# Kernel optimization log

Measured on AMD Instinct MI355X. Metric: run time of the kernel, lower is better.

## Reference

```python
import jax, jax.numpy as jnp
import numpy as np

N_NODES = 100000
N_EDGES = 1600000
IN_DIM = 128
LATENT = [128, 128, 16]  # last entry = num classes (logits dim)


def setup_inputs() -> dict:
    key = jax.random.key(0)
    ks = jax.random.split(key, 16)
    inp = {
        "x": jax.random.normal(ks[0], (N_NODES, IN_DIM), dtype=jnp.float32),
        "edge_index": jax.random.randint(ks[1], (2, N_EDGES), 0, N_NODES, dtype=jnp.int64),
        "edge_weight": jax.random.uniform(ks[2], (N_EDGES,), dtype=jnp.float32),
    }
    dims = [IN_DIM] + LATENT
    for i in range(len(LATENT)):
        fan_in = dims[i]
        scale = 1.0 / np.sqrt(fan_in)
        inp[f"W{i}"] = jax.random.uniform(ks[3 + 2 * i], (dims[i], dims[i + 1]), minval=-scale, maxval=scale, dtype=jnp.float32)
        inp[f"b{i}"] = jax.random.uniform(ks[4 + 2 * i], (dims[i + 1],), minval=-scale, maxval=scale, dtype=jnp.float32)
        inp[f"eps{i}"] = jnp.zeros((), dtype=jnp.float32)  # GINConv train_eps init = 0
    return inp


def _gin_layer(x, W, b, eps, src, dst, edge_weight):
    # message: x_j (optionally scaled by edge weight), summed into target nodes
    msg = x[src]
    if edge_weight is not None:
        msg = msg * edge_weight[:, None]
    agg = jax.ops.segment_sum(msg, dst, num_segments=N_NODES)
    h = (1.0 + eps) * x + agg
    return jax.nn.relu(h @ W + b)  # MLP = Linear + ReLU


def _l2_normalize(x, eps=1e-12):
    norm = jnp.linalg.norm(x, axis=-1, keepdims=True)
    return x / jnp.maximum(norm, eps)


def reference(x, edge_index, edge_weight, W0, b0, eps0, W1, b1, eps1, W2, b2, eps2):
    src, dst = edge_index[0], edge_index[1]
    params = [(W0, b0, eps0), (W1, b1, eps1), (W2, b2, eps2)]
    h = x
    # all but last layer: GINConv(with edge_weight) -> l2 normalize -> ReLU
    for (W, b, e) in params[:-1]:
        h = _gin_layer(h, W, b, e, src, dst, edge_weight)
        h = _l2_normalize(h)  # emb_normlize=True
        h = jax.nn.relu(h)
    # last layer: GINConv WITHOUT edge_weight (forward passes only x, edge_index)
    W, b, e = params[-1]
    logits = _gin_layer(h, W, b, e, src, dst, None)
    probs = jax.nn.softmax(logits, axis=-1)
    return (logits, probs)
```

## Files before the change

kernel.cpp:

```cpp
#include <hip/hip_runtime.h>
#include <hip/hip_bf16.h>

#define N_NODES 100000
#define N_EDGES 1600000
#define DIM 128
#define ODIM 16
#define NB 782
#define PCHUNK 3200
#define PBLK 500
#define FCAP 2560
#define CB4 12500

typedef unsigned int uint32;
typedef float f32x2 __attribute__((ext_vector_type(2)));
typedef float f32x4 __attribute__((ext_vector_type(4)));
typedef short bf16x8 __attribute__((ext_vector_type(8)));
typedef uint32 u32x4 __attribute__((ext_vector_type(4)));
typedef uint32 u32x2 __attribute__((ext_vector_type(2)));

static __device__ __forceinline__ float bflo(uint32 p) { return __uint_as_float(p << 16); }
static __device__ __forceinline__ float bfhi(uint32 p) { return __uint_as_float(p & 0xFFFF0000u); }
static __device__ __forceinline__ unsigned short f2bf(float f) {
  __hip_bfloat16 h = __float2bfloat16(f);
  return *reinterpret_cast<unsigned short*>(&h);
}
static __device__ __forceinline__ uint32 pk2bf(float a, float b) {
  return (uint32)f2bf(a) | ((uint32)f2bf(b) << 16);
}

__global__ __launch_bounds__(256) void prep_kernel(
    const f32x4* __restrict__ x4, uint32* __restrict__ Xu,
    const float* __restrict__ W0, const float* __restrict__ W1,
    const float* __restrict__ W2,
    unsigned short* __restrict__ pW0, unsigned short* __restrict__ pW1,
    unsigned short* __restrict__ pW2,
    const int* __restrict__ dst, int* __restrict__ bcnt) {
  __shared__ int h[NB];
  int b = blockIdx.x;
  int tid = threadIdx.x;
  if (b < CB4) {
    int i = b * 256 + tid;
    f32x4 v = __builtin_nontemporal_load(x4 + i);
    u32x2 o = {pk2bf(v[0], v[1]), pk2bf(v[2], v[3])};
    *(u32x2*)(Xu + (size_t)i * 2) = o;
  } else if (b < CB4 + 128) {
    int wsel = (b - CB4) >> 6;
    int idx = ((b - CB4) & 63) * 256 + tid;
    int j = idx & 7, lane = (idx >> 3) & 63, nt = (idx >> 9) & 7, kc = idx >> 12;
    const float* W = wsel ? W1 : W0;
    unsigned short* pW = wsel ? pW1 : pW0;
    pW[idx] = f2bf(W[(kc * 32 + (lane >> 4) * 8 + j) * DIM + nt * 16 + (lane & 15)]);
  } else if (b < CB4 + 136) {
    int idx = (b - CB4 - 128) * 256 + tid;
    int j = idx & 7, lane = (idx >> 3) & 63, kc = idx >> 9;
    pW2[idx] = f2bf(W2[(kc * 32 + (lane >> 4) * 8 + j) * ODIM + (lane & 15)]);
  } else {
    for (int i = tid; i < NB; i += 256) h[i] = 0;
    __syncthreads();
    int e0 = (b - CB4 - 136) * PCHUNK;
    for (int i = tid; i < PCHUNK; i += 256)
      atomicAdd(&h[__builtin_nontemporal_load(dst + e0 + i) >> 7], 1);
    __syncthreads();
    for (int i = tid; i < NB; i += 256)
      if (h[i]) atomicAdd(&bcnt[i], h[i]);
  }
}

__global__ __launch_bounds__(512) void coarse_partition_kernel(
    const int* __restrict__ src, const int* __restrict__ dst,
    const float* __restrict__ ew, const int* __restrict__ bcnt,
    int* __restrict__ bcur, int2* __restrict__ epack) {
  __shared__ int hist[NB];
  __shared__ int base_a[NB];
  __shared__ int base_g[NB];
  __shared__ int lcur_a[NB];
  __shared__ int gbase_a[NB];
  __shared__ int2 stg[PCHUNK];
  __shared__ int gpos[PCHUNK];

  int tid = threadIdx.x;
  int e0 = blockIdx.x * PCHUNK;

  for (int i = tid; i < NB; i += 512) hist[i] = 0;
  __syncthreads();
  for (int i = tid; i < PCHUNK; i += 512) atomicAdd(&hist[dst[e0 + i] >> 7], 1);
  __syncthreads();

  if (tid < 64) {
    int run = 0, rung = 0;
#pragma unroll
    for (int c = 0; c < 13; c++) {
      int idx = c * 64 + tid;
      int v = (idx < NB) ? hist[idx] : 0;
      int vg = (idx < NB) ? bcnt[idx] : 0;
      int incl = v, inclg = vg;
#pragma unroll
      for (int off = 1; off < 64; off <<= 1) {
        int t1 = __shfl_up(incl, off, 64);
        int t2 = __shfl_up(inclg, off, 64);
        if (tid >= off) { incl += t1; inclg += t2; }
      }
      if (idx < NB) {
        base_a[idx] = run + incl - v;
        base_g[idx] = rung + inclg - vg;
      }
      run += __shfl(incl, 63, 64);
      rung += __shfl(inclg, 63, 64);
    }
  }
  __syncthreads();
  for (int i = tid; i < NB; i += 512) {
    int c = hist[i];
    gbase_a[i] = (c > 0) ? base_g[i] + atomicAdd(&bcur[i], c) : 0;
    lcur_a[i] = base_a[i];
  }
  __syncthreads();

  for (int i = tid; i < PCHUNK; i += 512) {
    int e = e0 + i;
    int s = __builtin_nontemporal_load(src + e);
    int d = dst[e];
    float w = __builtin_nontemporal_load(ew + e);
    int bkt = d >> 7;
    int pos = atomicAdd(&lcur_a[bkt], 1);
    stg[pos] = make_int2(s | ((d & 127) << 20), __float_as_int(w));
    gpos[pos] = gbase_a[bkt] + (pos - base_a[bkt]);
  }
  __syncthreads();
  for (int i = tid; i < PCHUNK; i += 512) epack[gpos[i]] = stg[i];
}

__global__ __launch_bounds__(512) void fine_sort_kernel(
    const int* __restrict__ bcnt, int2* __restrict__ epack,
    int* __restrict__ row_ptr) {
  __shared__ int2 ebuf[FCAP];
  __shared__ unsigned short inv[FCAP];
  __shared__ int hist[128];
  __shared__ int sc[128];
  __shared__ int cur[128];
  __shared__ int redc[8];
  int tid = threadIdx.x;
  int b = blockIdx.x;
  int node0 = b << 7;

  int part = 0;
  for (int i = tid; i < b; i += 512) part += bcnt[i];
#pragma unroll
  for (int off = 32; off >= 1; off >>= 1) part += __shfl_xor(part, off, 64);
  if ((tid & 63) == 0) redc[tid >> 6] = part;
  if (tid < 128) hist[tid] = 0;
  __syncthreads();
  int lo = redc[0] + redc[1] + redc[2] + redc[3] +
           redc[4] + redc[5] + redc[6] + redc[7];
  int n = bcnt[b];
  if (n > FCAP) n = FCAP;

  for (int i = tid; i < n; i += 512) {
    int2 e = epack[lo + i];
    ebuf[i] = e;
    atomicAdd(&hist[(e.x >> 20) & 127], 1);
  }
  __syncthreads();
  if (tid < 64) {
    int run = 0;
#pragma unroll
    for (int c = 0; c < 2; c++) {
      int idx = c * 64 + tid;
      int v = hist[idx];
      int incl = v;
#pragma unroll
      for (int off = 1; off < 64; off <<= 1) {
        int tv = __shfl_up(incl, off, 64);
        if (tid >= off) incl += tv;
      }
      sc[idx] = run + incl;
      run += __shfl(incl, 63, 64);
    }
  }
  __syncthreads();
  if (tid < 128) {
    int excl = sc[tid] - hist[tid];
    if (node0 + tid < N_NODES) row_ptr[node0 + tid] = lo + excl;
    cur[tid] = excl;
  }
  if (b == 0 && tid == 0) row_ptr[N_NODES] = N_EDGES;
  __syncthreads();
  for (int i = tid; i < n; i += 512) {
    int p = atomicAdd(&cur[(ebuf[i].x >> 20) & 127], 1);
    inv[p] = (unsigned short)i;
  }
  __syncthreads();
  for (int p = tid; p < n; p += 512) {
    int2 e = ebuf[inv[p]];
    epack[lo + p] = make_int2(e.x & 0xFFFFF, e.y);
  }
}

__global__ __launch_bounds__(256, 8) void gather_bf16(
    const uint32* __restrict__ hu, const int* __restrict__ row_ptr,
    const int2* __restrict__ ep, const float* __restrict__ eps_p,
    uint32* __restrict__ cg) {
  int lane = threadIdx.x & 63;
  int node = blockIdx.x * 4 + (threadIdx.x >> 6);
  if (node >= N_NODES) return;
  int grp = lane >> 4, l4 = lane & 15;
  int a = row_ptr[node], bnd = row_ptr[node + 1];
  float epf = 1.0f + *eps_p;
  uint4 xv = *(const uint4*)(hu + (size_t)node * 64 + l4 * 4);
  f32x2 acc2[4];
#pragma unroll
  for (int k = 0; k < 4; k++) acc2[k] = (f32x2){0.f, 0.f};

  auto acc8 = [&](float wv, const uint4& p) {
    acc2[0] += (f32x2){bflo(p.x), bfhi(p.x)} * wv;
    acc2[1] += (f32x2){bflo(p.y), bfhi(p.y)} * wv;
    acc2[2] += (f32x2){bflo(p.z), bfhi(p.z)} * wv;
    acc2[3] += (f32x2){bflo(p.w), bfhi(p.w)} * wv;
  };

#pragma unroll 2
  for (int j = a; j < bnd; j += 16) {
    int i0 = j + grp;
    int i1 = i0 + 4;
    int i2 = i0 + 8;
    int i3 = i0 + 12;
    int2 e0 = ep[i0 < bnd ? i0 : a];
    int2 e1 = ep[i1 < bnd ? i1 : a];
    int2 e2 = ep[i2 < bnd ? i2 : a];
    int2 e3 = ep[i3 < bnd ? i3 : a];
    uint4 p0 = *(const uint4*)(hu + (size_t)e0.x * 64 + l4 * 4);
    uint4 p1 = *(const uint4*)(hu + (size_t)e1.x * 64 + l4 * 4);
    uint4 p2 = *(const uint4*)(hu + (size_t)e2.x * 64 + l4 * 4);
    uint4 p3 = *(const uint4*)(hu + (size_t)e3.x * 64 + l4 * 4);
    float w0 = i0 < bnd ? __int_as_float(e0.y) : 0.f;
    float w1 = i1 < bnd ? __int_as_float(e1.y) : 0.f;
    float w2 = i2 < bnd ? __int_as_float(e2.y) : 0.f;
    float w3 = i3 < bnd ? __int_as_float(e3.y) : 0.f;
    acc8(w0, p0);
    acc8(w1, p1);
    acc8(w2, p2);
    acc8(w3, p3);
  }
#pragma unroll
  for (int k = 0; k < 4; k++) {
    acc2[k].x += __shfl_xor(acc2[k].x, 16, 64);
    acc2[k].x += __shfl_xor(acc2[k].x, 32, 64);
    acc2[k].y += __shfl_xor(acc2[k].y, 16, 64);
    acc2[k].y += __shfl_xor(acc2[k].y, 32, 64);
  }
  if (lane < 16) {
    u32x4 st;
    st[0] = pk2bf(fmaf(epf, bflo(xv.x), acc2[0].x), fmaf(epf, bfhi(xv.x), acc2[0].y));
    st[1] = pk2bf(fmaf(epf, bflo(xv.y), acc2[1].x), fmaf(epf, bfhi(xv.y), acc2[1].y));
    st[2] = pk2bf(fmaf(epf, bflo(xv.z), acc2[2].x), fmaf(epf, bfhi(xv.z), acc2[2].y));
    st[3] = pk2bf(fmaf(epf, bflo(xv.w), acc2[3].x), fmaf(epf, bfhi(xv.w), acc2[3].y));
    __builtin_nontemporal_store(st, (u32x4*)(cg + (size_t)node * 64 + l4 * 4));
  }
}

template <int FUSE_PROJ>
__global__ __launch_bounds__(256) void gin_mlp_mfma(
    const uint32* __restrict__ Cu,
    const unsigned char* __restrict__ pW, const float* __restrict__ b,
    uint32* outH, const unsigned char* __restrict__ pW2,
    uint32* __restrict__ yb) {
  __shared__ __align__(16) unsigned char As[64 * 272];
  int tid = threadIdx.x;
  int node0 = blockIdx.x * 64;

  const uint4* C4 = (const uint4*)Cu;
#pragma unroll
  for (int c = 0; c < 4; c++) {
    int t = c * 256 + tid;
    int n = t >> 4, s = t & 15;
    int node = node0 + n;
    int cn = node < N_NODES ? node : N_NODES - 1;
    *(uint4*)(As + n * 272 + s * 16) = C4[(size_t)cn * 16 + s];
  }
  __syncthreads();

  int w = tid >> 6, l = tid & 63;
  int m = l & 15, q = l >> 4;

  f32x4 acc[8];
#pragma unroll
  for (int nt = 0; nt < 8; nt++) acc[nt] = (f32x4){0.f, 0.f, 0.f, 0.f};

  const unsigned char* Abase = As + (w * 16 + m) * 272 + q * 16;
#pragma unroll
  for (int kc = 0; kc < 4; kc++) {
    bf16x8 af = *(const bf16x8*)(Abase + kc * 64);
#pragma unroll
    for (int nt = 0; nt < 8; nt++) {
      bf16x8 bfr = *(const bf16x8*)(pW + (size_t)((kc * 8 + nt) * 64 + l) * 16);
      acc[nt] = __builtin_amdgcn_mfma_f32_16x16x32_bf16(af, bfr, acc[nt], 0, 0, 0);
    }
  }

  float ss[4] = {0.f, 0.f, 0.f, 0.f};
#pragma unroll
  for (int nt = 0; nt < 8; nt++) {
    float bj = b[nt * 16 + m];
#pragma unroll
    for (int r = 0; r < 4; r++) {
      float v = fmaxf(acc[nt][r] + bj, 0.0f);
      acc[nt][r] = v;
      ss[r] += v * v;
    }
  }
#pragma unroll
  for (int r = 0; r < 4; r++) {
    float s = ss[r];
    s += __shfl_xor(s, 1, 64);
    s += __shfl_xor(s, 2, 64);
    s += __shfl_xor(s, 4, 64);
    s += __shfl_xor(s, 8, 64);
    ss[r] = 1.0f / fmaxf(sqrtf(s), 1e-12f);
  }
#pragma unroll
  for (int nt = 0; nt < 8; nt++) {
#pragma unroll
    for (int r = 0; r < 4; r++) {
      unsigned short hv = f2bf(acc[nt][r] * ss[r]);
      *(unsigned short*)(As + (w * 16 + q * 4 + r) * 272 + (nt * 16 + m) * 2) = hv;
    }
  }

  if (FUSE_PROJ) {
    f32x4 accy = (f32x4){0.f, 0.f, 0.f, 0.f};
#pragma unroll
    for (int kc = 0; kc < 4; kc++) {
      bf16x8 af = *(const bf16x8*)(Abase + kc * 64);
      bf16x8 bfr = *(const bf16x8*)(pW2 + (size_t)(kc * 64 + l) * 16);
      accy = __builtin_amdgcn_mfma_f32_16x16x32_bf16(af, bfr, accy, 0, 0, 0);
    }
#pragma unroll
    for (int r = 0; r < 4; r++) {
      float v = accy[r];
      float o = __shfl_xor(v, 1, 64);
      if (!(m & 1)) {
        int orow = node0 + w * 16 + q * 4 + r;
        if (orow < N_NODES) yb[(size_t)orow * 8 + (m >> 1)] = pk2bf(v, o);
      }
    }
  } else {
    __syncthreads();
    int rem = N_NODES - node0; if (rem > 64) rem = 64;
    for (int i = tid; i < 1024; i += 256) {
      int row = i >> 4, seg = i & 15;
      if (row < rem) {
        uint4 vv = *(const uint4*)(As + row * 272 + seg * 16);
        *(uint4*)((unsigned char*)outH + (size_t)(node0 + row) * 256 + seg * 16) = vv;
      }
    }
  }
}

__global__ __launch_bounds__(256) void gather16_final_kernel(
    const uint32* __restrict__ yb, const int* __restrict__ row_ptr,
    const int2* __restrict__ ep, const float* __restrict__ bb,
    const float* __restrict__ eps_p, float* __restrict__ out_logits,
    float* __restrict__ out_probs) {
  int lane = threadIdx.x & 63;
  int node = blockIdx.x * 4 + (threadIdx.x >> 6);
  if (node >= N_NODES) return;
  int f2 = lane & 3;
  int eq = lane >> 2;
  int a = row_ptr[node], bnd = row_ptr[node + 1];
  f32x4 acc = (f32x4){0.f, 0.f, 0.f, 0.f};
  for (int j = a; j < bnd; j += 16) {
    int idx = j + eq;
    int vld = idx < bnd;
    int2 e = ep[vld ? idx : a];
    u32x2 p = *(const u32x2*)(yb + (size_t)e.x * 8 + f2 * 2);
    if (vld) {
      acc[0] += bflo(p[0]); acc[1] += bfhi(p[0]);
      acc[2] += bflo(p[1]); acc[3] += bfhi(p[1]);
    }
  }
#pragma unroll
  for (int k = 0; k < 4; k++) {
#pragma unroll
    for (int off = 4; off <= 32; off <<= 1)
      acc[k] += __shfl_xor(acc[k], off, 64);
  }
  if (eq == 0) {
    float epf = 1.0f + *eps_p;
    u32x2 ys = *(const u32x2*)(yb + (size_t)node * 8 + f2 * 2);
    f32x4 lg;
    lg[0] = fmaxf(fmaf(epf, bflo(ys[0]), acc[0]) + bb[f2 * 4 + 0], 0.f);
    lg[1] = fmaxf(fmaf(epf, bfhi(ys[0]), acc[1]) + bb[f2 * 4 + 1], 0.f);
    lg[2] = fmaxf(fmaf(epf, bflo(ys[1]), acc[2]) + bb[f2 * 4 + 2], 0.f);
    lg[3] = fmaxf(fmaf(epf, bfhi(ys[1]), acc[3]) + bb[f2 * 4 + 3], 0.f);
    float mx = fmaxf(fmaxf(lg[0], lg[1]), fmaxf(lg[2], lg[3]));
    mx = fmaxf(mx, __shfl_xor(mx, 1, 4));
    mx = fmaxf(mx, __shfl_xor(mx, 2, 4));
    f32x4 ex;
    float s = 0.f;
#pragma unroll
    for (int k = 0; k < 4; k++) { ex[k] = __expf(lg[k] - mx); s += ex[k]; }
    s += __shfl_xor(s, 1, 4);
    s += __shfl_xor(s, 2, 4);
    float invs = 1.0f / s;
    size_t base = (size_t)node * ODIM + f2 * 4;
    *(f32x4*)(out_logits + base) = lg;
    f32x4 pr = {ex[0] * invs, ex[1] * invs, ex[2] * invs, ex[3] * invs};
    *(f32x4*)(out_probs + base) = pr;
  }
}

extern "C" void kernel_launch(void* const* d_in, const int* in_sizes, int n_in,
                              void* d_out, int out_size, void* d_ws, size_t ws_size,
                              hipStream_t stream) {
  const float* x = (const float*)d_in[0];
  const int* ei = (const int*)d_in[1];
  const float* ew = (const float*)d_in[2];
  const float* W0 = (const float*)d_in[3];
  const float* b0 = (const float*)d_in[4];
  const float* e0 = (const float*)d_in[5];
  const float* W1 = (const float*)d_in[6];
  const float* b1 = (const float*)d_in[7];
  const float* e1 = (const float*)d_in[8];
  const float* W2 = (const float*)d_in[9];
  const float* b2 = (const float*)d_in[10];
  const float* e2 = (const float*)d_in[11];
  float* out = (float*)d_out;

  const int* srcp = ei;
  const int* dstp = ei + N_EDGES;

  char* ws = (char*)d_ws;
  size_t off = 0;
  uint32* Cg  = (uint32*)(ws + off);  off += (size_t)N_NODES * DIM * 2;
  uint32* Xb  = (uint32*)(ws + off);  off += (size_t)N_NODES * DIM * 2;
  uint32* H   = (uint32*)(ws + off);  off += (size_t)N_NODES * DIM * 2;
  int2* epack = (int2*)(ws + off);    off += (size_t)N_EDGES * 8;
  uint32* yb  = (uint32*)(ws + off);  off += (size_t)N_NODES * 8 * 4;
  int* row_ptr = (int*)(ws + off);    off += (size_t)(N_NODES + 16) * 4;
  int* bcnt   = (int*)(ws + off);     off += 4096;
  int* bcur   = (int*)(ws + off);     off += 4096;
  unsigned short* pW0 = (unsigned short*)(ws + off); off += 32768;
  unsigned short* pW1 = (unsigned short*)(ws + off); off += 32768;
  unsigned short* pW2 = (unsigned short*)(ws + off); off += 4096;

  hipMemsetAsync(bcnt, 0, 8192, stream);
  prep_kernel<<<CB4 + 136 + PBLK, 256, 0, stream>>>(
      (const f32x4*)x, Xb, W0, W1, W2, pW0, pW1, pW2, dstp, bcnt);

  coarse_partition_kernel<<<PBLK, 512, 0, stream>>>(srcp, dstp, ew, bcnt, bcur, epack);
  fine_sort_kernel<<<NB, 512, 0, stream>>>(bcnt, epack, row_ptr);

  int ggrid = (N_NODES + 3) / 4;
  int mgrid = (N_NODES + 63) / 64;

  gather_bf16<<<ggrid, 256, 0, stream>>>(Xb, row_ptr, epack, e0, Cg);
  gin_mlp_mfma<0><<<mgrid, 256, 0, stream>>>(Cg, (const unsigned char*)pW0, b0,
                                             H, nullptr, nullptr);
  gather_bf16<<<ggrid, 256, 0, stream>>>(H, row_ptr, epack, e1, Cg);
  gin_mlp_mfma<1><<<mgrid, 256, 0, stream>>>(Cg, (const unsigned char*)pW1, b1,
                                             nullptr, (const unsigned char*)pW2, yb);
  gather16_final_kernel<<<ggrid, 256, 0, stream>>>(yb, row_ptr, epack, b2, e2,
                                                   out, out + (size_t)N_NODES * ODIM);
}
```

Before: 358.0 us.

## Replace exact bucket offsets with fixed-capacity padded buckets, dropping the histogram pass

Removes the separate per-bucket histogram pass over dst, the memset, and the global prefix sums. Instead, each coarse bucket gets a fixed slot of FCAP entries in an oversized edge buffer, and CSR uses separate row_ptr/row_end arrays. This saves a full read of dst and several scans, at the cost of a larger, sparser edge buffer. It relies on no bucket exceeding FCAP edges (overflow is silently truncated), which holds for uniform random indices but is an input-distribution assumption.

```diff
diff --git a/kernel.cpp b/kernel.cpp
--- a/kernel.cpp
+++ b/kernel.cpp
@@ -33,9 +33,7 @@
     const float* __restrict__ W0, const float* __restrict__ W1,
     const float* __restrict__ W2,
     unsigned short* __restrict__ pW0, unsigned short* __restrict__ pW1,
-    unsigned short* __restrict__ pW2,
-    const int* __restrict__ dst, int* __restrict__ bcnt) {
-  __shared__ int h[NB];
+    unsigned short* __restrict__ pW2, int* __restrict__ bcur) {
   int b = blockIdx.x;
   int tid = threadIdx.x;
   if (b < CB4) {
@@ -55,24 +53,16 @@
     int j = idx & 7, lane = (idx >> 3) & 63, kc = idx >> 9;
     pW2[idx] = f2bf(W2[(kc * 32 + (lane >> 4) * 8 + j) * ODIM + (lane & 15)]);
   } else {
-    for (int i = tid; i < NB; i += 256) h[i] = 0;
-    __syncthreads();
-    int e0 = (b - CB4 - 136) * PCHUNK;
-    for (int i = tid; i < PCHUNK; i += 256)
-      atomicAdd(&h[__builtin_nontemporal_load(dst + e0 + i) >> 7], 1);
-    __syncthreads();
-    for (int i = tid; i < NB; i += 256)
-      if (h[i]) atomicAdd(&bcnt[i], h[i]);
+    for (int i = tid; i < NB; i += 256) bcur[i] = 0;
   }
 }
 
 __global__ __launch_bounds__(512) void coarse_partition_kernel(
     const int* __restrict__ src, const int* __restrict__ dst,
-    const float* __restrict__ ew, const int* __restrict__ bcnt,
+    const float* __restrict__ ew,
     int* __restrict__ bcur, int2* __restrict__ epack) {
   __shared__ int hist[NB];
   __shared__ int base_a[NB];
-  __shared__ int base_g[NB];
   __shared__ int lcur_a[NB];
   __shared__ int gbase_a[NB];
   __shared__ int2 stg[PCHUNK];
@@ -87,31 +77,25 @@
   __syncthreads();
 
   if (tid < 64) {
-    int run = 0, rung = 0;
+    int run = 0;
 #pragma unroll
     for (int c = 0; c < 13; c++) {
       int idx = c * 64 + tid;
       int v = (idx < NB) ? hist[idx] : 0;
-      int vg = (idx < NB) ? bcnt[idx] : 0;
-      int incl = v, inclg = vg;
+      int incl = v;
 #pragma unroll
       for (int off = 1; off < 64; off <<= 1) {
         int t1 = __shfl_up(incl, off, 64);
-        int t2 = __shfl_up(inclg, off, 64);
-        if (tid >= off) { incl += t1; inclg += t2; }
+        if (tid >= off) incl += t1;
       }
-      if (idx < NB) {
-        base_a[idx] = run + incl - v;
-        base_g[idx] = rung + inclg - vg;
-      }
+      if (idx < NB) base_a[idx] = run + incl - v;
       run += __shfl(incl, 63, 64);
-      rung += __shfl(inclg, 63, 64);
     }
   }
   __syncthreads();
   for (int i = tid; i < NB; i += 512) {
     int c = hist[i];
-    gbase_a[i] = (c > 0) ? base_g[i] + atomicAdd(&bcur[i], c) : 0;
+    gbase_a[i] = (c > 0) ? i * FCAP + atomicAdd(&bcur[i], c) : 0;
     lcur_a[i] = base_a[i];
   }
   __syncthreads();
@@ -131,28 +115,21 @@
 }
 
 __global__ __launch_bounds__(512) void fine_sort_kernel(
-    const int* __restrict__ bcnt, int2* __restrict__ epack,
-    int* __restrict__ row_ptr) {
+    const int* __restrict__ bcur, int2* __restrict__ epack,
+    int* __restrict__ row_ptr, int* __restrict__ row_end) {
   __shared__ int2 ebuf[FCAP];
   __shared__ unsigned short inv[FCAP];
   __shared__ int hist[128];
   __shared__ int sc[128];
   __shared__ int cur[128];
-  __shared__ int redc[8];
   int tid = threadIdx.x;
   int b = blockIdx.x;
   int node0 = b << 7;
-
-  int part = 0;
-  for (int i = tid; i < b; i += 512) part += bcnt[i];
-#pragma unroll
-  for (int off = 32; off >= 1; off >>= 1) part += __shfl_xor(part, off, 64);
-  if ((tid & 63) == 0) redc[tid >> 6] = part;
+  int lo = b * FCAP;
+
   if (tid < 128) hist[tid] = 0;
   __syncthreads();
-  int lo = redc[0] + redc[1] + redc[2] + redc[3] +
-           redc[4] + redc[5] + redc[6] + redc[7];
-  int n = bcnt[b];
+  int n = bcur[b];
   if (n > FCAP) n = FCAP;
 
   for (int i = tid; i < n; i += 512) {
@@ -179,11 +156,13 @@
   }
   __syncthreads();
   if (tid < 128) {
-    int excl = sc[tid] - hist[tid];
-    if (node0 + tid < N_NODES) row_ptr[node0 + tid] = lo + excl;
-    cur[tid] = excl;
-  }
-  if (b == 0 && tid == 0) row_ptr[N_NODES] = N_EDGES;
+    int node = node0 + tid;
+    if (node < N_NODES) {
+      row_ptr[node] = lo + sc[tid] - hist[tid];
+      row_end[node] = lo + sc[tid];
+    }
+    cur[tid] = sc[tid] - hist[tid];
+  }
   __syncthreads();
   for (int i = tid; i < n; i += 512) {
     int p = atomicAdd(&cur[(ebuf[i].x >> 20) & 127], 1);
@@ -198,13 +177,13 @@
 
 __global__ __launch_bounds__(256, 8) void gather_bf16(
     const uint32* __restrict__ hu, const int* __restrict__ row_ptr,
-    const int2* __restrict__ ep, const float* __restrict__ eps_p,
-    uint32* __restrict__ cg) {
+    const int* __restrict__ row_end, const int2* __restrict__ ep,
+    const float* __restrict__ eps_p, uint32* __restrict__ cg) {
   int lane = threadIdx.x & 63;
   int node = blockIdx.x * 4 + (threadIdx.x >> 6);
   if (node >= N_NODES) return;
   int grp = lane >> 4, l4 = lane & 15;
-  int a = row_ptr[node], bnd = row_ptr[node + 1];
+  int a = row_ptr[node], bnd = row_end[node];
   float epf = 1.0f + *eps_p;
   uint4 xv = *(const uint4*)(hu + (size_t)node * 64 + l4 * 4);
   f32x2 acc2[4];
@@ -358,15 +337,15 @@
 
 __global__ __launch_bounds__(256) void gather16_final_kernel(
     const uint32* __restrict__ yb, const int* __restrict__ row_ptr,
-    const int2* __restrict__ ep, const float* __restrict__ bb,
-    const float* __restrict__ eps_p, float* __restrict__ out_logits,
-    float* __restrict__ out_probs) {
+    const int* __restrict__ row_end, const int2* __restrict__ ep,
+    const float* __restrict__ bb, const float* __restrict__ eps_p,
+    float* __restrict__ out_logits, float* __restrict__ out_probs) {
   int lane = threadIdx.x & 63;
   int node = blockIdx.x * 4 + (threadIdx.x >> 6);
   if (node >= N_NODES) return;
   int f2 = lane & 3;
   int eq = lane >> 2;
-  int a = row_ptr[node], bnd = row_ptr[node + 1];
+  int a = row_ptr[node], bnd = row_end[node];
   f32x4 acc = (f32x4){0.f, 0.f, 0.f, 0.f};
   for (int j = a; j < bnd; j += 16) {
     int idx = j + eq;
@@ -434,31 +413,31 @@
   uint32* Cg  = (uint32*)(ws + off);  off += (size_t)N_NODES * DIM * 2;
   uint32* Xb  = (uint32*)(ws + off);  off += (size_t)N_NODES * DIM * 2;
   uint32* H   = (uint32*)(ws + off);  off += (size_t)N_NODES * DIM * 2;
-  int2* epack = (int2*)(ws + off);    off += (size_t)N_EDGES * 8;
+  int2* epack = (int2*)(ws + off);    off += (size_t)NB * FCAP * 8 + 8192;
   uint32* yb  = (uint32*)(ws + off);  off += (size_t)N_NODES * 8 * 4;
   int* row_ptr = (int*)(ws + off);    off += (size_t)(N_NODES + 16) * 4;
-  int* bcnt   = (int*)(ws + off);     off += 4096;
+  int* row_end = (int*)(ws + off);    off += (size_t)(N_NODES + 16) * 4;
   int* bcur   = (int*)(ws + off);     off += 4096;
   unsigned short* pW0 = (unsigned short*)(ws + off); off += 32768;
   unsigned short* pW1 = (unsigned short*)(ws + off); off += 32768;
   unsigned short* pW2 = (unsigned short*)(ws + off); off += 4096;
 
-  hipMemsetAsync(bcnt, 0, 8192, stream);
-  prep_kernel<<<CB4 + 136 + PBLK, 256, 0, stream>>>(
-      (const f32x4*)x, Xb, W0, W1, W2, pW0, pW1, pW2, dstp, bcnt);
-
-  coarse_partition_kernel<<<PBLK, 512, 0, stream>>>(srcp, dstp, ew, bcnt, bcur, epack);
-  fine_sort_kernel<<<NB, 512, 0, stream>>>(bcnt, epack, row_ptr);
+  prep_kernel<<<CB4 + 137, 256, 0, stream>>>(
+      (const f32x4*)x, Xb, W0, W1, W2, pW0, pW1, pW2, bcur);
+
+  coarse_partition_kernel<<<PBLK, 512, 0, stream>>>(srcp, dstp, ew, bcur, epack);
+  fine_sort_kernel<<<NB, 512, 0, stream>>>(bcur, epack, row_ptr, row_end);
 
   int ggrid = (N_NODES + 3) / 4;
   int mgrid = (N_NODES + 63) / 64;
 
-  gather_bf16<<<ggrid, 256, 0, stream>>>(Xb, row_ptr, epack, e0, Cg);
+  gather_bf16<<<ggrid, 256, 0, stream>>>(Xb, row_ptr, row_end, epack, e0, Cg);
   gin_mlp_mfma<0><<<mgrid, 256, 0, stream>>>(Cg, (const unsigned char*)pW0, b0,
                                              H, nullptr, nullptr);
-  gather_bf16<<<ggrid, 256, 0, stream>>>(H, row_ptr, epack, e1, Cg);
+  gather_bf16<<<ggrid, 256, 0, stream>>>(H, row_ptr, row_end, epack, e1, Cg);
   gin_mlp_mfma<1><<<mgrid, 256, 0, stream>>>(Cg, (const unsigned char*)pW1, b1,
                                              nullptr, (const unsigned char*)pW2, yb);
-  gather16_final_kernel<<<ggrid, 256, 0, stream>>>(yb, row_ptr, epack, b2, e2,
-                                                   out, out + (size_t)N_NODES * ODIM);
-}
+  gather16_final_kernel<<<ggrid, 256, 0, stream>>>(yb, row_ptr, row_end, epack,
+                                                   b2, e2, out,
+                                                   out + (size_t)N_NODES * ODIM);
+}
```

After: 342.2 us. 1.05x faster.
